# Kernel optimization log

Hardware: AMD Instinct MI355X
Metric: run time of the kernel (lower is better)

The kernel has to match this reference:

```python
import jax, jax.numpy as jnp
import numpy as np

D_MODEL = 1024
N_HEADS = 16
D_K = 64
CHUNK_LEN = 64


def setup_inputs() -> dict:
    key = jax.random.key(0)
    ks = jax.random.split(key, 10)
    B, S = 4, 2048
    NC, NN, NL = 32, 2, 128
    s = 1.0 / np.sqrt(D_MODEL)
    inp = {
        "query": jax.random.normal(ks[0], (B, S, D_MODEL), dtype=jnp.float32),
        "key": jax.random.normal(ks[1], (B, NC, NN, NL, D_MODEL), dtype=jnp.float32),
        # Linear weights stored as [in, out] (equivalent to torch W.T)
        "Wq": jax.random.normal(ks[2], (D_MODEL, N_HEADS * D_K), dtype=jnp.float32) * s,
        "bq": jnp.zeros((N_HEADS * D_K,), dtype=jnp.float32),
        "Wk": jax.random.normal(ks[3], (D_MODEL, N_HEADS * D_K), dtype=jnp.float32) * s,
        "bk": jnp.zeros((N_HEADS * D_K,), dtype=jnp.float32),
        "Wv": jax.random.normal(ks[4], (D_MODEL, N_HEADS * D_K), dtype=jnp.float32) * s,
        "bv": jnp.zeros((N_HEADS * D_K,), dtype=jnp.float32),
        "Wo": jax.random.normal(ks[5], (N_HEADS * D_K, D_MODEL), dtype=jnp.float32) * s,
        "bo": jnp.zeros((D_MODEL,), dtype=jnp.float32),
    }
    return inp


def reference(query, key, Wq, bq, Wk, bk, Wv, bv, Wo, bo):
    B, S, D = query.shape
    _, NC, NN, NL, _ = key.shape
    L = NN * NL  # kv length per chunk
    # reshape query into chunks: [B, NC, chunk_len, D]
    q_in = query.reshape(B, NC, CHUNK_LEN, D)
    kv_in = key.reshape(B, NC, L, D)  # key used for both K and V in the original
    # projections, split heads: [B, NC, H, T, d_k]
    q = (q_in @ Wq + bq).reshape(B, NC, CHUNK_LEN, N_HEADS, D_K).transpose(0, 1, 3, 2, 4)
    k = (kv_in @ Wk + bk).reshape(B, NC, L, N_HEADS, D_K).transpose(0, 1, 3, 2, 4)
    v = (kv_in @ Wv + bv).reshape(B, NC, L, N_HEADS, D_K).transpose(0, 1, 3, 2, 4)
    # attention per (batch, chunk, head)
    scores = jnp.einsum("bchqd,bchkd->bchqk", q, k) / jnp.sqrt(jnp.float32(D_K))
    attn = jax.nn.softmax(scores, axis=-1)
    o = jnp.einsum("bchqk,bchkd->bchqd", attn, v)
    # merge heads: [B, NC, chunk_len, H*d_k]
    o = o.transpose(0, 1, 3, 2, 4).reshape(B, NC, CHUNK_LEN, N_HEADS * D_K)
    out = o @ Wo + bo
    return out.reshape(B, S, D)
```

## Files before the change

### kernel.cpp

```cpp
#include <hip/hip_runtime.h>
#include <hip/hip_bf16.h>
#include <stdint.h>

#define DMODEL 1024
#define NHEADS 16
#define DK 64
#define TQ 64
#define LKV 256
#define MQ 8192
#define MKV 32768

typedef __bf16 bf16x8 __attribute__((ext_vector_type(8)));
typedef float f32x4 __attribute__((ext_vector_type(4)));
typedef unsigned short u16x8 __attribute__((ext_vector_type(8)));
typedef unsigned short u16;

__device__ __forceinline__ unsigned short f2bf(float f) {
    union { float f; unsigned int i; } x; x.f = f;
    unsigned int r = (x.i + 0x7FFFu + ((x.i >> 16) & 1u)) >> 16;
    return (unsigned short)r;
}

__device__ __forceinline__ void gload_lds16(const void* g, void* l) {
    __builtin_amdgcn_global_load_lds(
        (const __attribute__((address_space(1))) unsigned int*)g,
        (__attribute__((address_space(3))) unsigned int*)l, 16, 0, 0);
}

__global__ __launch_bounds__(256) void cvt_f32_bf16(const float* __restrict__ in,
                                                    unsigned short* __restrict__ out) {
    long long i = ((long long)blockIdx.x * 256 + threadIdx.x) * 8;
    f32x4 a = *(const f32x4*)(in + i);
    f32x4 b = *(const f32x4*)(in + i + 4);
    u16x8 o;
    o[0] = f2bf(a[0]); o[1] = f2bf(a[1]); o[2] = f2bf(a[2]); o[3] = f2bf(a[3]);
    o[4] = f2bf(b[0]); o[5] = f2bf(b[1]); o[6] = f2bf(b[2]); o[7] = f2bf(b[3]);
    *(u16x8*)(out + i) = o;
}

__global__ __launch_bounds__(256) void transpose_w_cvt4(const float* __restrict__ w0,
                                                        const float* __restrict__ w1,
                                                        const float* __restrict__ w2,
                                                        const float* __restrict__ w3,
                                                        u16* __restrict__ o0,
                                                        u16* __restrict__ o1,
                                                        u16* __restrict__ o2,
                                                        u16* __restrict__ o3) {
    __shared__ float tile[64][65];
    const float* in; u16* out;
    switch (blockIdx.z) {
        case 0: in = w0; out = o0; break;
        case 1: in = w1; out = o1; break;
        case 2: in = w2; out = o2; break;
        default: in = w3; out = o3; break;
    }
    int bi = blockIdx.y, bj = blockIdx.x;
    int tid = threadIdx.x;
    int c = tid & 63, r0 = tid >> 6;
#pragma unroll
    for (int p = 0; p < 16; ++p) {
        int r = r0 + 4 * p;
        tile[r][c] = in[(size_t)(bi * 64 + r) * 1024 + bj * 64 + c];
    }
    __syncthreads();
#pragma unroll
    for (int p = 0; p < 16; ++p) {
        int r = r0 + 4 * p;
        out[(size_t)(bj * 64 + r) * 1024 + bi * 64 + c] = f2bf(tile[c][r]);
    }
}

template <int OUTMODE>
__global__ __launch_bounds__(256) void gemm_bias(const u16* __restrict__ A,
                                                 const u16* __restrict__ Bt,
                                                 const float* __restrict__ bias,
                                                 void* __restrict__ OutV) {
    __shared__ alignas(16) u16 aLds[128 * 32];
    __shared__ alignas(16) u16 bLds[128 * 32];

    int tid = threadIdx.x;
    int lane = tid & 63, wid = tid >> 6;
    int m0 = blockIdx.x * 128;
    int n0 = blockIdx.y * 128;
    int wr = (wid >> 1) * 64, wc = (wid & 1) * 64;

    f32x4 zero = {0.f, 0.f, 0.f, 0.f};
    f32x4 acc[4][4];
#pragma unroll
    for (int i = 0; i < 4; ++i)
#pragma unroll
        for (int j = 0; j < 4; ++j) acc[i][j] = zero;

    int sr = lane >> 2;
    int sk = (lane & 3) * 8;
    const u16* aG = A + (size_t)(m0 + sr) * 1024 + sk;
    const u16* bG = Bt + (size_t)(n0 + sr) * 1024 + sk;
    int c0 = wid, c1 = wid + 4;

    int fr = lane & 15, fg = (lane >> 4) * 8;

    for (int kt = 0; kt < 1024; kt += 32) {
        gload_lds16(aG + (size_t)(c0 * 16) * 1024 + kt, aLds + c0 * 512);
        gload_lds16(aG + (size_t)(c1 * 16) * 1024 + kt, aLds + c1 * 512);
        gload_lds16(bG + (size_t)(c0 * 16) * 1024 + kt, bLds + c0 * 512);
        gload_lds16(bG + (size_t)(c1 * 16) * 1024 + kt, bLds + c1 * 512);
        __syncthreads();

        bf16x8 af[4], bf[4];
#pragma unroll
        for (int mt = 0; mt < 4; ++mt)
            af[mt] = *(const bf16x8*)&aLds[(wr + mt * 16 + fr) * 32 + fg];
#pragma unroll
        for (int nt = 0; nt < 4; ++nt)
            bf[nt] = *(const bf16x8*)&bLds[(wc + nt * 16 + fr) * 32 + fg];
#pragma unroll
        for (int mt = 0; mt < 4; ++mt)
#pragma unroll
            for (int nt = 0; nt < 4; ++nt)
                acc[mt][nt] = __builtin_amdgcn_mfma_f32_16x16x32_bf16(af[mt], bf[nt], acc[mt][nt], 0, 0, 0);
        __syncthreads();
    }

    float bv[4];
#pragma unroll
    for (int nt = 0; nt < 4; ++nt) bv[nt] = bias[n0 + wc + nt * 16 + fr];

    if (OUTMODE == 0) {
        u16* Out = (u16*)OutV;
#pragma unroll
        for (int mt = 0; mt < 4; ++mt)
#pragma unroll
            for (int r = 0; r < 4; ++r) {
                size_t row = (size_t)(m0 + wr + mt * 16 + (lane >> 4) * 4 + r);
#pragma unroll
                for (int nt = 0; nt < 4; ++nt)
                    Out[row * 1024 + n0 + wc + nt * 16 + fr] = f2bf(acc[mt][nt][r] + bv[nt]);
            }
    } else {
        float* Out = (float*)OutV;
#pragma unroll
        for (int mt = 0; mt < 4; ++mt)
#pragma unroll
            for (int r = 0; r < 4; ++r) {
                size_t row = (size_t)(m0 + wr + mt * 16 + (lane >> 4) * 4 + r);
#pragma unroll
                for (int nt = 0; nt < 4; ++nt)
                    Out[row * 1024 + n0 + wc + nt * 16 + fr] = acc[mt][nt][r] + bv[nt];
            }
    }
}


__device__ __forceinline__ void stageA64(const u16* src, u16* ldsTile, int row0, int tid) {
    int w = tid >> 6, l = tid & 63;
    int r = row0 + w * 8 + (l >> 3);
    int k16 = (l & 7) ^ ((l >> 3) & 7);
    gload_lds16(src + (size_t)r * 1024 + k16 * 8, ldsTile + (size_t)(row0 + w * 8) * 64);
}
__device__ __forceinline__ void stageB64(const u16* src, u16* ldsTile, int j, int odd, int tid) {
    int w = tid >> 6, l = tid & 63;
    int ib = j * 64 + w * 8;
    int rowbase = ((ib >> 5) << 6) + (ib & 31) + (odd ? 32 : 0);
    int r = rowbase + (l >> 3);
    int k16 = (l & 7) ^ ((l >> 3) & 7);
    gload_lds16(src + (size_t)r * 1024 + k16 * 8, ldsTile + (size_t)rowbase * 64);
}

#define SBAR() do { __builtin_amdgcn_s_barrier(); asm volatile("" ::: "memory"); } while (0)
#define VMWAIT0() asm volatile("s_waitcnt vmcnt(0)" ::: "memory")

__global__ __launch_bounds__(512, 2) void proj_fused(const u16* __restrict__ Akv,
                                                     const u16* __restrict__ Aq,
                                                     const u16* __restrict__ WkT,
                                                     const u16* __restrict__ WvT,
                                                     const u16* __restrict__ WqT,
                                                     const float* __restrict__ bk,
                                                     const float* __restrict__ bv,
                                                     const float* __restrict__ bq,
                                                     u16* __restrict__ Kp,
                                                     u16* __restrict__ Vt,
                                                     u16* __restrict__ Qp,
                                                     int nmKV, int nmQ) {
    __shared__ alignas(16) u16 lds[65536];
    u16* ldsA0 = lds;          u16* ldsA1 = lds + 16384;
    u16* ldsB0 = lds + 32768;  u16* ldsB1 = lds + 49152;

    int tid = threadIdx.x, lane = tid & 63, wid = tid >> 6;
    int wm = wid >> 2, wn = wid & 3;

    int nB = gridDim.x;
    int bid = blockIdx.x;
    int qq = nB >> 3, rr = nB & 7;
    int xcd = bid & 7, idx = bid >> 3;
    int wg = (xcd < rr) ? xcd * (qq + 1) + idx : rr * (qq + 1) + (xcd - rr) * qq + idx;

    const u16* A; const u16* B; const float* bias; u16* Out; int mode;
    int nKV4 = nmKV * 4;
    int lwg;
    if (wg < nKV4)            { lwg = wg;            A = Akv; B = WkT; bias = bk; Out = Kp; mode = 0; }
    else if (wg < 2 * nKV4)   { lwg = wg - nKV4;     A = Akv; B = WvT; bias = bv; Out = Vt; mode = 1; }
    else                      { lwg = wg - 2 * nKV4; A = Aq;  B = WqT; bias = bq; Out = Qp; mode = 0; }
    int m0 = (lwg >> 2) * 256;
    int n0 = (lwg & 3) * 256;

    const u16* aSrc = A + (size_t)m0 * 1024;
    const u16* bSrc = B + (size_t)n0 * 1024;

    f32x4 zero = {0.f, 0.f, 0.f, 0.f};
    f32x4 acc[8][4];
#pragma unroll
    for (int i = 0; i < 8; ++i)
#pragma unroll
        for (int j = 0; j < 4; ++j) acc[i][j] = zero;

    bf16x8 aR[4][2], b0R[2][2], b1R[2][2];

#define READ_A(lA, half)                                                         \
    do {                                                                         \
        _Pragma("unroll") for (int mf = 0; mf < 4; ++mf) {                       \
            int row = wm * 128 + (half) * 64 + mf * 16 + (lane & 15);            \
            _Pragma("unroll") for (int kk = 0; kk < 2; ++kk) {                   \
                int k16 = kk * 4 + (lane >> 4);                                  \
                aR[mf][kk] = *(const bf16x8*)&(lA)[row * 64 + ((k16 ^ (row & 7)) << 3)]; \
            }                                                                    \
        }                                                                        \
    } while (0)
#define READ_B(lB, half, dst)                                                    \
    do {                                                                         \
        _Pragma("unroll") for (int nf = 0; nf < 2; ++nf) {                       \
            int row = wn * 64 + (half) * 32 + nf * 16 + (lane & 15);             \
            _Pragma("unroll") for (int kk = 0; kk < 2; ++kk) {                   \
                int k16 = kk * 4 + (lane >> 4);                                  \
                dst[nf][kk] = *(const bf16x8*)&(lB)[row * 64 + ((k16 ^ (row & 7)) << 3)]; \
            }                                                                    \
        }                                                                        \
    } while (0)
#define MFMA16(mh, nh, bR)                                                       \
    do {                                                                         \
        __builtin_amdgcn_s_setprio(1);                                           \
        _Pragma("unroll") for (int mf = 0; mf < 4; ++mf)                         \
            _Pragma("unroll") for (int nf = 0; nf < 2; ++nf)                     \
                _Pragma("unroll") for (int kk = 0; kk < 2; ++kk)                 \
                    acc[(mh)*4 + mf][(nh)*2 + nf] =                              \
                        __builtin_amdgcn_mfma_f32_16x16x32_bf16(                 \
                            aR[mf][kk], bR[nf][kk], acc[(mh)*4 + mf][(nh)*2 + nf], 0, 0, 0); \
        __builtin_amdgcn_s_setprio(0);                                           \
    } while (0)

    stageA64(aSrc, ldsA0, 0, tid);    stageA64(aSrc, ldsA0, 128, tid);
    stageB64(bSrc, ldsB0, 0, 0, tid); stageB64(bSrc, ldsB0, 1, 0, tid);
    stageB64(bSrc, ldsB0, 0, 1, tid); stageB64(bSrc, ldsB0, 1, 1, tid);
    stageA64(aSrc, ldsA0, 64, tid);   stageA64(aSrc, ldsA0, 192, tid);
    VMWAIT0();
    SBAR();

    for (int t = 0; t < 16; ++t) {
        int cur = t & 1;
        u16* lA = cur ? ldsA1 : ldsA0;
        u16* lB = cur ? ldsB1 : ldsB0;
        u16* pA = cur ? ldsA0 : ldsA1;
        u16* pB = cur ? ldsB0 : ldsB1;
        const u16* aNext = aSrc + (t + 1) * 64;
        const u16* bNext = bSrc + (t + 1) * 64;
        bool pf = (t < 15);

        READ_A(lA, 0);
        READ_B(lB, 0, b0R);
        if (pf) {
            stageA64(aNext, pA, 0, tid);    stageA64(aNext, pA, 128, tid);
            stageB64(bNext, pB, 0, 0, tid); stageB64(bNext, pB, 1, 0, tid);
        }
        MFMA16(0, 0, b0R);

        READ_B(lB, 1, b1R);
        if (pf) {
            stageB64(bNext, pB, 0, 1, tid); stageB64(bNext, pB, 1, 1, tid);
            stageA64(aNext, pA, 64, tid);   stageA64(aNext, pA, 192, tid);
        }
        MFMA16(0, 1, b1R);

        READ_A(lA, 1);
        MFMA16(1, 1, b1R);

        MFMA16(1, 0, b0R);

        VMWAIT0();
        SBAR();
    }

    float bvv[4];
#pragma unroll
    for (int NF = 0; NF < 4; ++NF) bvv[NF] = bias[n0 + wn * 64 + NF * 16 + (lane & 15)];

    if (mode == 0) {
#pragma unroll
        for (int MF = 0; MF < 8; ++MF)
#pragma unroll
            for (int r = 0; r < 4; ++r) {
                size_t row = (size_t)(m0 + wm * 128 + MF * 16 + (lane >> 4) * 4 + r);
#pragma unroll
                for (int NF = 0; NF < 4; ++NF)
                    Out[row * 1024 + n0 + wn * 64 + NF * 16 + (lane & 15)] =
                        f2bf(acc[MF][NF][r] + bvv[NF]);
            }
    } else {
#pragma unroll
        for (int MF = 0; MF < 8; ++MF)
#pragma unroll
            for (int r = 0; r < 4; ++r) {
                int gm = m0 + wm * 128 + MF * 16 + (lane >> 4) * 4 + r;
                int bc2 = gm >> 8, lv = gm & 255;
#pragma unroll
                for (int NF = 0; NF < 4; ++NF) {
                    int n = n0 + wn * 64 + NF * 16 + (lane & 15);
                    int hh = n >> 6, dd = n & 63;
                    Out[(size_t)((bc2 * 16 + hh) * 64 + dd) * 256 + lv] =
                        f2bf(acc[MF][NF][r] + bvv[NF]);
                }
            }
    }
#undef READ_A
#undef READ_B
#undef MFMA16
}

__global__ __launch_bounds__(256) void attn_kernel(const u16* __restrict__ Q,
                                                   const u16* __restrict__ K,
                                                   const u16* __restrict__ Vt,
                                                   u16* O) {
    __shared__ alignas(16) u16 pLds[64 * 264];

    int tid = threadIdx.x;
    int lane = tid & 63, w = tid >> 6;
    int bc = blockIdx.x >> 4, h = blockIdx.x & 15;
    int fr = lane & 15, g = lane >> 4;

    const u16* qb = Q + (size_t)(bc * 64 + w * 16 + fr) * 1024 + h * 64 + g * 8;
    bf16x8 qf0 = *(const bf16x8*)qb;
    bf16x8 qf1 = *(const bf16x8*)(qb + 32);

    const u16* kb = K + (size_t)(bc * 256 + fr) * 1024 + h * 64 + g * 8;

    f32x4 zero = {0.f, 0.f, 0.f, 0.f};
    f32x4 sc[16];
#pragma unroll
    for (int nt = 0; nt < 16; ++nt) sc[nt] = zero;

#pragma unroll
    for (int nt = 0; nt < 16; ++nt) {
        bf16x8 kf0 = *(const bf16x8*)(kb + (size_t)(nt * 16) * 1024);
        bf16x8 kf1 = *(const bf16x8*)(kb + (size_t)(nt * 16) * 1024 + 32);
        sc[nt] = __builtin_amdgcn_mfma_f32_16x16x32_bf16(qf0, kf0, sc[nt], 0, 0, 0);
        sc[nt] = __builtin_amdgcn_mfma_f32_16x16x32_bf16(qf1, kf1, sc[nt], 0, 0, 0);
    }

    const float scale = 0.125f;
    float mx[4], sum[4];
#pragma unroll
    for (int r = 0; r < 4; ++r) {
        float m = -1e30f;
#pragma unroll
        for (int nt = 0; nt < 16; ++nt) {
            sc[nt][r] *= scale;
            m = fmaxf(m, sc[nt][r]);
        }
#pragma unroll
        for (int x = 1; x < 16; x <<= 1) m = fmaxf(m, __shfl_xor(m, x, 64));
        mx[r] = m;
        sum[r] = 0.f;
    }
#pragma unroll
    for (int nt = 0; nt < 16; ++nt)
#pragma unroll
        for (int r = 0; r < 4; ++r) {
            float p = __expf(sc[nt][r] - mx[r]);
            sum[r] += p;
            pLds[(w * 16 + g * 4 + r) * 264 + nt * 16 + fr] = f2bf(p);
        }
#pragma unroll
    for (int r = 0; r < 4; ++r)
#pragma unroll
        for (int x = 1; x < 16; x <<= 1) sum[r] += __shfl_xor(sum[r], x, 64);

    __syncthreads();

    f32x4 oa[4];
#pragma unroll
    for (int nt = 0; nt < 4; ++nt) oa[nt] = zero;

    const u16* vtb = Vt + (size_t)((bc * 16 + h) * 64) * 256;
#pragma unroll
    for (int ks = 0; ks < 8; ++ks) {
        bf16x8 pf = *(const bf16x8*)&pLds[(w * 16 + fr) * 264 + ks * 32 + g * 8];
#pragma unroll
        for (int nt = 0; nt < 4; ++nt) {
            bf16x8 vf = *(const bf16x8*)(vtb + (size_t)(nt * 16 + fr) * 256 + ks * 32 + g * 8);
            oa[nt] = __builtin_amdgcn_mfma_f32_16x16x32_bf16(pf, vf, oa[nt], 0, 0, 0);
        }
    }

    float rs[4];
#pragma unroll
    for (int r = 0; r < 4; ++r) rs[r] = 1.0f / sum[r];

    u16* ob = O + (size_t)(bc * 64 + w * 16 + g * 4) * 1024 + h * 64 + fr;
#pragma unroll
    for (int nt = 0; nt < 4; ++nt)
#pragma unroll
        for (int r = 0; r < 4; ++r)
            ob[(size_t)r * 1024 + nt * 16] = f2bf(oa[nt][r] * rs[r]);
}

extern "C" void kernel_launch(void* const* d_in, const int* in_sizes, int n_in,
                              void* d_out, int out_size, void* d_ws, size_t ws_size,
                              hipStream_t stream) {
    const float* query = (const float*)d_in[0];
    const float* keyin = (const float*)d_in[1];
    const float* Wq = (const float*)d_in[2];
    const float* bq = (const float*)d_in[3];
    const float* Wk = (const float*)d_in[4];
    const float* bk = (const float*)d_in[5];
    const float* Wv = (const float*)d_in[6];
    const float* bv = (const float*)d_in[7];
    const float* Wo = (const float*)d_in[8];
    const float* bo = (const float*)d_in[9];

    u16* ws = (u16*)d_ws;
    const size_t MB1 = 1024 * 1024;

    u16* WqT = ws;
    u16* WkT = ws + MB1;
    u16* WvT = ws + 2 * MB1;
    u16* WoT = ws + 3 * MB1;
    u16* qb16 = ws + 4 * MB1;
    u16* Qp   = qb16 + (size_t)MQ * 1024;
    u16* kvb  = Qp + (size_t)MQ * 1024;

    size_t ws_elems = ws_size / 2;
    size_t fixed = 4 * MB1 + 2 * (size_t)MQ * 1024;
    size_t avail = (ws_elems > fixed) ? (ws_elems - fixed) : 0;
    long long max_rows = (long long)(avail / (3 * 1024));
    int slice_rows = (int)((max_rows / 256) * 256);
    if (slice_rows >= MKV) slice_rows = MKV;
    else if (slice_rows >= 16384) slice_rows = 16384;
    if (slice_rows < 256) slice_rows = 256;

    u16* Kp = kvb + (size_t)slice_rows * 1024;
    u16* Vt = Kp + (size_t)slice_rows * 1024;

    dim3 tb(256);
    transpose_w_cvt4<<<dim3(16, 16, 4), tb, 0, stream>>>(Wq, Wk, Wv, Wo, WqT, WkT, WvT, WoT);
    cvt_f32_bf16<<<dim3(MQ * 1024 / (256 * 8)), tb, 0, stream>>>(query, qb16);

    for (int r0 = 0; r0 < MKV; r0 += slice_rows) {
        int rows = MKV - r0;
        if (rows > slice_rows) rows = slice_rows;
        cvt_f32_bf16<<<dim3(rows * 1024 / (256 * 8)), tb, 0, stream>>>(
            keyin + (size_t)r0 * 1024, kvb);
        int nmKV = rows / 256;
        int nmQ = (r0 == 0) ? (MQ / 256) : 0;
        proj_fused<<<dim3(nmKV * 8 + nmQ * 4), dim3(512), 0, stream>>>(
            kvb, qb16, WkT, WvT, WqT, bk, bv, bq, Kp, Vt, Qp, nmKV, nmQ);
        size_t qoff = (size_t)(r0 / 4) * 1024;
        attn_kernel<<<dim3((rows / 256) * 16), tb, 0, stream>>>(
            Qp + qoff, Kp, Vt, Qp + qoff);
    }

    gemm_bias<2><<<dim3(MQ / 128, 8), tb, 0, stream>>>(Qp, WoT, bo, d_out);
}
```

Before: 315.7 us.

## Restructure projection GEMM main loop into four barrier-synced phases with partial vmcnt waits

Replaces the projection GEMM's per-tile schedule with four phases. Each phase reads one k-half of A/B fragments, issues two prefetch loads, waits on a partial vmcnt, crosses a barrier, then runs the MFMAs. The global-to-LDS staging now waits only on the loads it needs (vmcnt(2)/vmcnt(4)) rather than draining all loads at the end of each iteration, and fragment registers shrink to reduce register pressure. This adds many more barriers per k-step and relies on careful vmcnt accounting, which risks stalls or races if the counts do not match the issue order.

```diff
diff --git a/kernel.cpp b/kernel.cpp
--- a/kernel.cpp
+++ b/kernel.cpp
@@ -151,23 +151,15 @@
 }
 
 
-__device__ __forceinline__ void stageA64(const u16* src, u16* ldsTile, int row0, int tid) {
+__device__ __forceinline__ void stage64(const u16* src, u16* ldsTile, int row0, int tid) {
     int w = tid >> 6, l = tid & 63;
     int r = row0 + w * 8 + (l >> 3);
     int k16 = (l & 7) ^ ((l >> 3) & 7);
     gload_lds16(src + (size_t)r * 1024 + k16 * 8, ldsTile + (size_t)(row0 + w * 8) * 64);
 }
-__device__ __forceinline__ void stageB64(const u16* src, u16* ldsTile, int j, int odd, int tid) {
-    int w = tid >> 6, l = tid & 63;
-    int ib = j * 64 + w * 8;
-    int rowbase = ((ib >> 5) << 6) + (ib & 31) + (odd ? 32 : 0);
-    int r = rowbase + (l >> 3);
-    int k16 = (l & 7) ^ ((l >> 3) & 7);
-    gload_lds16(src + (size_t)r * 1024 + k16 * 8, ldsTile + (size_t)rowbase * 64);
-}
-
-#define SBAR() do { __builtin_amdgcn_s_barrier(); asm volatile("" ::: "memory"); } while (0)
-#define VMWAIT0() asm volatile("s_waitcnt vmcnt(0)" ::: "memory")
+
+#define SBAR()  do { __builtin_amdgcn_s_barrier(); asm volatile("" ::: "memory"); } while (0)
+#define LGKM0() asm volatile("s_waitcnt lgkmcnt(0)" ::: "memory")
 
 __global__ __launch_bounds__(512, 2) void proj_fused(const u16* __restrict__ Akv,
                                                      const u16* __restrict__ Aq,
@@ -213,45 +205,50 @@
 #pragma unroll
         for (int j = 0; j < 4; ++j) acc[i][j] = zero;
 
-    bf16x8 aR[4][2], b0R[2][2], b1R[2][2];
-
-#define READ_A(lA, half)                                                         \
+    bf16x8 aF[4], bF[2];
+
+#define READ_Q(lA, lB, mh, nh, kk)                                               \
     do {                                                                         \
         _Pragma("unroll") for (int mf = 0; mf < 4; ++mf) {                       \
-            int row = wm * 128 + (half) * 64 + mf * 16 + (lane & 15);            \
-            _Pragma("unroll") for (int kk = 0; kk < 2; ++kk) {                   \
-                int k16 = kk * 4 + (lane >> 4);                                  \
-                aR[mf][kk] = *(const bf16x8*)&(lA)[row * 64 + ((k16 ^ (row & 7)) << 3)]; \
-            }                                                                    \
+            int row = wm * 128 + (mh) * 64 + mf * 16 + (lane & 15);              \
+            int k16 = (kk) * 4 + (lane >> 4);                                    \
+            aF[mf] = *(const bf16x8*)&(lA)[row * 64 + ((k16 ^ (row & 7)) << 3)]; \
+        }                                                                        \
+        _Pragma("unroll") for (int nf = 0; nf < 2; ++nf) {                       \
+            int row = wn * 64 + (nh) * 32 + nf * 16 + (lane & 15);               \
+            int k16 = (kk) * 4 + (lane >> 4);                                    \
+            bF[nf] = *(const bf16x8*)&(lB)[row * 64 + ((k16 ^ (row & 7)) << 3)]; \
         }                                                                        \
     } while (0)
-#define READ_B(lB, half, dst)                                                    \
+#define MFMA8(mh, nh)                                                            \
     do {                                                                         \
-        _Pragma("unroll") for (int nf = 0; nf < 2; ++nf) {                       \
-            int row = wn * 64 + (half) * 32 + nf * 16 + (lane & 15);             \
-            _Pragma("unroll") for (int kk = 0; kk < 2; ++kk) {                   \
-                int k16 = kk * 4 + (lane >> 4);                                  \
-                dst[nf][kk] = *(const bf16x8*)&(lB)[row * 64 + ((k16 ^ (row & 7)) << 3)]; \
-            }                                                                    \
-        }                                                                        \
-    } while (0)
-#define MFMA16(mh, nh, bR)                                                       \
-    do {                                                                         \
-        __builtin_amdgcn_s_setprio(1);                                           \
         _Pragma("unroll") for (int mf = 0; mf < 4; ++mf)                         \
             _Pragma("unroll") for (int nf = 0; nf < 2; ++nf)                     \
-                _Pragma("unroll") for (int kk = 0; kk < 2; ++kk)                 \
-                    acc[(mh)*4 + mf][(nh)*2 + nf] =                              \
-                        __builtin_amdgcn_mfma_f32_16x16x32_bf16(                 \
-                            aR[mf][kk], bR[nf][kk], acc[(mh)*4 + mf][(nh)*2 + nf], 0, 0, 0); \
+                acc[(mh)*4 + mf][(nh)*2 + nf] =                                  \
+                    __builtin_amdgcn_mfma_f32_16x16x32_bf16(                     \
+                        aF[mf], bF[nf], acc[(mh)*4 + mf][(nh)*2 + nf], 0, 0, 0); \
+    } while (0)
+#define PHASE(lA, lB, mh, nh, STAGES, WAITS)                                     \
+    do {                                                                         \
+        READ_Q(lA, lB, mh, nh, 0);                                               \
+        STAGES;                                                                  \
+        WAITS;                                                                   \
+        SBAR();                                                                  \
+        LGKM0();                                                                 \
+        __builtin_amdgcn_s_setprio(1);                                           \
+        MFMA8(mh, nh);                                                           \
+        READ_Q(lA, lB, mh, nh, 1);                                               \
+        LGKM0();                                                                 \
+        MFMA8(mh, nh);                                                           \
         __builtin_amdgcn_s_setprio(0);                                           \
+        SBAR();                                                                  \
     } while (0)
 
-    stageA64(aSrc, ldsA0, 0, tid);    stageA64(aSrc, ldsA0, 128, tid);
-    stageB64(bSrc, ldsB0, 0, 0, tid); stageB64(bSrc, ldsB0, 1, 0, tid);
-    stageB64(bSrc, ldsB0, 0, 1, tid); stageB64(bSrc, ldsB0, 1, 1, tid);
-    stageA64(aSrc, ldsA0, 64, tid);   stageA64(aSrc, ldsA0, 192, tid);
-    VMWAIT0();
+    stage64(bSrc, ldsB0, 0, tid);   stage64(bSrc, ldsB0, 64, tid);
+    stage64(bSrc, ldsB0, 128, tid); stage64(bSrc, ldsB0, 192, tid);
+    stage64(aSrc, ldsA0, 0, tid);   stage64(aSrc, ldsA0, 128, tid);
+    stage64(aSrc, ldsA0, 64, tid);  stage64(aSrc, ldsA0, 192, tid);
+    asm volatile("s_waitcnt vmcnt(2)" ::: "memory");
     SBAR();
 
     for (int t = 0; t < 16; ++t) {
@@ -260,32 +257,26 @@
         u16* lB = cur ? ldsB1 : ldsB0;
         u16* pA = cur ? ldsA0 : ldsA1;
         u16* pB = cur ? ldsB0 : ldsB1;
-        const u16* aNext = aSrc + (t + 1) * 64;
-        const u16* bNext = bSrc + (t + 1) * 64;
+        const u16* aN = aSrc + (t + 1) * 64;
+        const u16* bN = bSrc + (t + 1) * 64;
         bool pf = (t < 15);
 
-        READ_A(lA, 0);
-        READ_B(lB, 0, b0R);
-        if (pf) {
-            stageA64(aNext, pA, 0, tid);    stageA64(aNext, pA, 128, tid);
-            stageB64(bNext, pB, 0, 0, tid); stageB64(bNext, pB, 1, 0, tid);
-        }
-        MFMA16(0, 0, b0R);
-
-        READ_B(lB, 1, b1R);
-        if (pf) {
-            stageB64(bNext, pB, 0, 1, tid); stageB64(bNext, pB, 1, 1, tid);
-            stageA64(aNext, pA, 64, tid);   stageA64(aNext, pA, 192, tid);
-        }
-        MFMA16(0, 1, b1R);
-
-        READ_A(lA, 1);
-        MFMA16(1, 1, b1R);
-
-        MFMA16(1, 0, b0R);
-
-        VMWAIT0();
-        SBAR();
+        PHASE(lA, lB, 0, 0,
+              { if (pf) { stage64(bN, pB, 0, tid); stage64(bN, pB, 64, tid); } },
+              {});
+
+        PHASE(lA, lB, 0, 1,
+              { if (pf) { stage64(bN, pB, 128, tid); stage64(bN, pB, 192, tid); } },
+              { if (pf) { asm volatile("s_waitcnt vmcnt(4)" ::: "memory"); }
+                else    { asm volatile("s_waitcnt vmcnt(0)" ::: "memory"); } });
+
+        PHASE(lA, lB, 1, 1,
+              { if (pf) { stage64(aN, pA, 0, tid); stage64(aN, pA, 128, tid); } },
+              {});
+
+        PHASE(lA, lB, 1, 0,
+              { if (pf) { stage64(aN, pA, 64, tid); stage64(aN, pA, 192, tid); } },
+              { if (pf) { asm volatile("s_waitcnt vmcnt(2)" ::: "memory"); } });
     }
 
     float bvv[4];
@@ -319,9 +310,9 @@
                 }
             }
     }
-#undef READ_A
-#undef READ_B
-#undef MFMA16
+#undef READ_Q
+#undef MFMA8
+#undef PHASE
 }
 
 __global__ __launch_bounds__(256) void attn_kernel(const u16* __restrict__ Q,
```

Measured after the change: 335.3 us. 6.2% more time.

## Triple-buffer B tiles with two-ahead prefetch and split Q projection across slices

Applied to the files above, without the earlier changes.

The projection GEMM now keeps three LDS buffers for the weight (B) tile and prefetches it two iterations ahead, while A stays double-buffered. The end-of-iteration wait becomes vmcnt(4) instead of a full drain, so global loads can stay in flight across the barrier. The B staging is simplified to a plain contiguous row layout. On the host, the Q projection is spread over KV slices in proportion to each slice's rows instead of all running in the first slice, and slice size is rounded to 1024 rows. LDS use grows from 128KB to 160KB per block, which may limit occupancy at two blocks per CU.

```diff
diff --git a/kernel.cpp b/kernel.cpp
--- a/kernel.cpp
+++ b/kernel.cpp
@@ -151,23 +151,14 @@
 }
 
 
-__device__ __forceinline__ void stageA64(const u16* src, u16* ldsTile, int row0, int tid) {
+__device__ __forceinline__ void stage64(const u16* src, u16* ldsTile, int row0, int tid) {
     int w = tid >> 6, l = tid & 63;
     int r = row0 + w * 8 + (l >> 3);
     int k16 = (l & 7) ^ ((l >> 3) & 7);
     gload_lds16(src + (size_t)r * 1024 + k16 * 8, ldsTile + (size_t)(row0 + w * 8) * 64);
 }
-__device__ __forceinline__ void stageB64(const u16* src, u16* ldsTile, int j, int odd, int tid) {
-    int w = tid >> 6, l = tid & 63;
-    int ib = j * 64 + w * 8;
-    int rowbase = ((ib >> 5) << 6) + (ib & 31) + (odd ? 32 : 0);
-    int r = rowbase + (l >> 3);
-    int k16 = (l & 7) ^ ((l >> 3) & 7);
-    gload_lds16(src + (size_t)r * 1024 + k16 * 8, ldsTile + (size_t)rowbase * 64);
-}
 
 #define SBAR() do { __builtin_amdgcn_s_barrier(); asm volatile("" ::: "memory"); } while (0)
-#define VMWAIT0() asm volatile("s_waitcnt vmcnt(0)" ::: "memory")
 
 __global__ __launch_bounds__(512, 2) void proj_fused(const u16* __restrict__ Akv,
                                                      const u16* __restrict__ Aq,
@@ -181,9 +172,10 @@
                                                      u16* __restrict__ Vt,
                                                      u16* __restrict__ Qp,
                                                      int nmKV, int nmQ) {
-    __shared__ alignas(16) u16 lds[65536];
-    u16* ldsA0 = lds;          u16* ldsA1 = lds + 16384;
-    u16* ldsB0 = lds + 32768;  u16* ldsB1 = lds + 49152;
+    __shared__ alignas(16) u16 lds[81920];
+    u16* ldsA0 = lds;
+    u16* ldsA1 = lds + 16384;
+    u16* ldsB  = lds + 32768;
 
     int tid = threadIdx.x, lane = tid & 63, wid = tid >> 6;
     int wm = wid >> 2, wn = wid & 3;
@@ -247,45 +239,46 @@
         __builtin_amdgcn_s_setprio(0);                                           \
     } while (0)
 
-    stageA64(aSrc, ldsA0, 0, tid);    stageA64(aSrc, ldsA0, 128, tid);
-    stageB64(bSrc, ldsB0, 0, 0, tid); stageB64(bSrc, ldsB0, 1, 0, tid);
-    stageB64(bSrc, ldsB0, 0, 1, tid); stageB64(bSrc, ldsB0, 1, 1, tid);
-    stageA64(aSrc, ldsA0, 64, tid);   stageA64(aSrc, ldsA0, 192, tid);
-    VMWAIT0();
+    stage64(bSrc, ldsB, 0, tid);          stage64(bSrc, ldsB, 64, tid);
+    stage64(bSrc, ldsB, 128, tid);        stage64(bSrc, ldsB, 192, tid);
+    stage64(aSrc, ldsA0, 0, tid);         stage64(aSrc, ldsA0, 64, tid);
+    stage64(aSrc, ldsA0, 128, tid);       stage64(aSrc, ldsA0, 192, tid);
+    stage64(bSrc + 64, ldsB + 16384, 0, tid);   stage64(bSrc + 64, ldsB + 16384, 64, tid);
+    stage64(bSrc + 64, ldsB + 16384, 128, tid); stage64(bSrc + 64, ldsB + 16384, 192, tid);
+    asm volatile("s_waitcnt vmcnt(4)" ::: "memory");
     SBAR();
 
+    int bi = 0;
     for (int t = 0; t < 16; ++t) {
-        int cur = t & 1;
-        u16* lA = cur ? ldsA1 : ldsA0;
-        u16* lB = cur ? ldsB1 : ldsB0;
-        u16* pA = cur ? ldsA0 : ldsA1;
-        u16* pB = cur ? ldsB0 : ldsB1;
-        const u16* aNext = aSrc + (t + 1) * 64;
-        const u16* bNext = bSrc + (t + 1) * 64;
-        bool pf = (t < 15);
+        u16* lA = (t & 1) ? ldsA1 : ldsA0;
+        u16* lB = ldsB + bi * 16384;
+        u16* pA = (t & 1) ? ldsA0 : ldsA1;
+        int bi2 = bi + 2; if (bi2 >= 3) bi2 -= 3;
+        u16* pB = ldsB + bi2 * 16384;
+        const u16* aN = aSrc + (t + 1) * 64;
+        const u16* bN2 = bSrc + (t + 2) * 64;
+        bool pfA = (t < 15), pfB = (t < 14);
 
         READ_A(lA, 0);
         READ_B(lB, 0, b0R);
-        if (pf) {
-            stageA64(aNext, pA, 0, tid);    stageA64(aNext, pA, 128, tid);
-            stageB64(bNext, pB, 0, 0, tid); stageB64(bNext, pB, 1, 0, tid);
-        }
+        if (pfA) { stage64(aN, pA, 0, tid); stage64(aN, pA, 128, tid); }
         MFMA16(0, 0, b0R);
 
         READ_B(lB, 1, b1R);
-        if (pf) {
-            stageB64(bNext, pB, 0, 1, tid); stageB64(bNext, pB, 1, 1, tid);
-            stageA64(aNext, pA, 64, tid);   stageA64(aNext, pA, 192, tid);
-        }
+        if (pfA) { stage64(aN, pA, 64, tid); stage64(aN, pA, 192, tid); }
         MFMA16(0, 1, b1R);
 
         READ_A(lA, 1);
+        if (pfB) { stage64(bN2, pB, 0, tid); stage64(bN2, pB, 64, tid); }
         MFMA16(1, 1, b1R);
 
+        if (pfB) { stage64(bN2, pB, 128, tid); stage64(bN2, pB, 192, tid); }
         MFMA16(1, 0, b0R);
 
-        VMWAIT0();
-        SBAR();
+        if (t < 14)      { asm volatile("s_waitcnt vmcnt(4)" ::: "memory"); SBAR(); }
+        else if (t == 14){ asm volatile("s_waitcnt vmcnt(0)" ::: "memory"); SBAR(); }
+
+        bi = bi + 1; if (bi >= 3) bi -= 3;
     }
 
     float bvv[4];
@@ -440,10 +433,10 @@
     size_t fixed = 4 * MB1 + 2 * (size_t)MQ * 1024;
     size_t avail = (ws_elems > fixed) ? (ws_elems - fixed) : 0;
     long long max_rows = (long long)(avail / (3 * 1024));
-    int slice_rows = (int)((max_rows / 256) * 256);
+    int slice_rows = (int)((max_rows / 1024) * 1024);
     if (slice_rows >= MKV) slice_rows = MKV;
     else if (slice_rows >= 16384) slice_rows = 16384;
-    if (slice_rows < 256) slice_rows = 256;
+    if (slice_rows < 1024) slice_rows = 1024;
 
     u16* Kp = kvb + (size_t)slice_rows * 1024;
     u16* Vt = Kp + (size_t)slice_rows * 1024;
@@ -452,18 +445,22 @@
     transpose_w_cvt4<<<dim3(16, 16, 4), tb, 0, stream>>>(Wq, Wk, Wv, Wo, WqT, WkT, WvT, WoT);
     cvt_f32_bf16<<<dim3(MQ * 1024 / (256 * 8)), tb, 0, stream>>>(query, qb16);
 
+    int qdone = 0;
     for (int r0 = 0; r0 < MKV; r0 += slice_rows) {
         int rows = MKV - r0;
         if (rows > slice_rows) rows = slice_rows;
         cvt_f32_bf16<<<dim3(rows * 1024 / (256 * 8)), tb, 0, stream>>>(
             keyin + (size_t)r0 * 1024, kvb);
         int nmKV = rows / 256;
-        int nmQ = (r0 == 0) ? (MQ / 256) : 0;
+        int nmQ = rows / 1024;
         proj_fused<<<dim3(nmKV * 8 + nmQ * 4), dim3(512), 0, stream>>>(
-            kvb, qb16, WkT, WvT, WqT, bk, bv, bq, Kp, Vt, Qp, nmKV, nmQ);
+            kvb, qb16 + (size_t)qdone * 256 * 1024,
+            WkT, WvT, WqT, bk, bv, bq,
+            Kp, Vt, Qp + (size_t)qdone * 256 * 1024, nmKV, nmQ);
         size_t qoff = (size_t)(r0 / 4) * 1024;
         attn_kernel<<<dim3((rows / 256) * 16), tb, 0, stream>>>(
             Qp + qoff, Kp, Vt, Qp + qoff);
+        qdone += nmQ;
     }
 
     gemm_bias<2><<<dim3(MQ / 128, 8), tb, 0, stream>>>(Qp, WoT, bo, d_out);
```

Result: no change. 316.3 us (+0.2%).
